# Kernel optimization log

Measured on AMD Instinct MI355X. Metric: run time of the kernel, lower is better.

The kernel has to match this reference:

```python
import jax, jax.numpy as jnp
import numpy as np

N = 50000        # num nodes
E = 800000       # num edges
F_IN = 128
H1 = 256
H2 = 256
C = 64


def _sage_conv(x, edge_index, W_l, b_l, W_r):
    """PyG SAGEConv (mean aggr): lin_l(mean over in-neighbors of x_j) + lin_r(x)."""
    src = edge_index[0]
    dst = edge_index[1]
    n = x.shape[0]
    # gather messages [E, d] then segment-mean into [N, d]
    agg = jax.ops.segment_sum(x[src], dst, num_segments=n)
    cnt = jax.ops.segment_sum(jnp.ones((edge_index.shape[1],), x.dtype), dst, num_segments=n)
    mean = agg / jnp.maximum(cnt, 1.0)[:, None]
    return mean @ W_l + b_l + x @ W_r


def setup_inputs() -> dict:
    key = jax.random.key(0)
    ks = jax.random.split(key, 10)
    x = jax.random.normal(ks[0], (N, F_IN), dtype=jnp.float32)
    edge_index = jax.random.randint(ks[1], (2, E), 0, N, dtype=jnp.int64)
    s1 = 1.0 / np.sqrt(F_IN)
    s2 = 1.0 / np.sqrt(H1)
    s3 = 1.0 / np.sqrt(H2)
    return {
        "x": x,
        "edge_index": edge_index,
        "W1_l": jax.random.uniform(ks[2], (F_IN, H1), jnp.float32, -s1, s1),
        "b1": jnp.zeros((H1,), jnp.float32),
        "W1_r": jax.random.uniform(ks[3], (F_IN, H1), jnp.float32, -s1, s1),
        "W2_l": jax.random.uniform(ks[4], (H1, H2), jnp.float32, -s2, s2),
        "b2": jnp.zeros((H2,), jnp.float32),
        "W2_r": jax.random.uniform(ks[5], (H1, H2), jnp.float32, -s2, s2),
        "Wc": jax.random.uniform(ks[6], (H2, C), jnp.float32, -s3, s3),
        "bc": jax.random.uniform(ks[7], (C,), jnp.float32, -s3, s3),
    }


def reference(x, edge_index, W1_l, b1, W1_r, W2_l, b2, W2_r, Wc, bc):
    # inference mode: dropout is identity
    h = jax.nn.relu(_sage_conv(x, edge_index, W1_l, b1, W1_r))
    h = jax.nn.relu(_sage_conv(h, edge_index, W2_l, b2, W2_r))
    return h @ Wc + bc
```

## Files before the change

kernel.cpp:

```cpp
#include <hip/hip_runtime.h>
#include <hip/hip_bf16.h>


#define F_IN 128
#define H1_DIM 256
#define H2_DIM 256
#define C_DIM 64

typedef __attribute__((ext_vector_type(8))) short bf16x8;
typedef __attribute__((ext_vector_type(8))) unsigned short u16x8;
typedef __attribute__((ext_vector_type(4))) float f32x4;

__device__ __forceinline__ unsigned short f2bf(float f) {
    unsigned u = __builtin_bit_cast(unsigned, f);
    u = (u + 0x7FFFu + ((u >> 16) & 1u)) >> 16;
    return (unsigned short)u;
}
__device__ __forceinline__ float bf2f(unsigned short h) {
    return __builtin_bit_cast(float, (unsigned)h << 16);
}

__global__ void k_detect(const unsigned int* __restrict__ ei, int* __restrict__ flag) {
    if (blockIdx.x == 0 && threadIdx.x == 0) {
        int is64 = 1;
        for (int i = 1; i < 256; i += 2) {
            if (ei[i] != 0u) { is64 = 0; break; }
        }
        *flag = is64;
    }
}

__device__ __forceinline__ int ei_at(const void* ei, const int* flag, long long idx) {
    return (*flag) ? (int)((const long long*)ei)[idx] : ((const int*)ei)[idx];
}

__global__ void k_degree(const void* __restrict__ ei, const int* __restrict__ flag,
                         int* __restrict__ cnt, int E) {
    int i = blockIdx.x * blockDim.x + threadIdx.x;
    if (i >= E) return;
    atomicAdd(&cnt[ei_at(ei, flag, (long long)E + i)], 1);
}

__global__ void k_scan1(const int* __restrict__ cnt, int* __restrict__ rowptr,
                        int* __restrict__ bsum, int n) {
    __shared__ int s[256];
    int i = blockIdx.x * 256 + threadIdx.x;
    int v = (i < n) ? cnt[i] : 0;
    s[threadIdx.x] = v;
    __syncthreads();
    for (int off = 1; off < 256; off <<= 1) {
        int t = (threadIdx.x >= off) ? s[threadIdx.x - off] : 0;
        __syncthreads();
        s[threadIdx.x] += t;
        __syncthreads();
    }
    if (i < n) rowptr[i] = s[threadIdx.x] - v;
    if (threadIdx.x == 255) bsum[blockIdx.x] = s[255];
}

__global__ void k_scan2(const int* __restrict__ bsum, int* __restrict__ boff, int nb) {
    __shared__ int s[1024];
    int t = threadIdx.x;
    int v = (t < nb) ? bsum[t] : 0;
    s[t] = v;
    __syncthreads();
    for (int off = 1; off < 1024; off <<= 1) {
        int u = (t >= off) ? s[t - off] : 0;
        __syncthreads();
        s[t] += u;
        __syncthreads();
    }
    if (t < nb) boff[t] = s[t] - v;
}

__global__ void k_scan3(int* __restrict__ rowptr, const int* __restrict__ boff,
                        int n, int total) {
    int i = blockIdx.x * 256 + threadIdx.x;
    if (i < n) rowptr[i] += boff[i >> 8];
    if (i == 0) rowptr[n] = total;
}

__global__ void k_scatter(const void* __restrict__ ei, const int* __restrict__ flag,
                          const int* __restrict__ rowptr, int* __restrict__ pos,
                          int* __restrict__ col, int E) {
    int i = blockIdx.x * blockDim.x + threadIdx.x;
    if (i >= E) return;
    int s = ei_at(ei, flag, i);
    int d = ei_at(ei, flag, (long long)E + i);
    int p = atomicAdd(&pos[d], 1);
    col[rowptr[d] + p] = s;
}

__global__ void k_prep_x(const float* __restrict__ x, unsigned short* __restrict__ hi,
                         unsigned short* __restrict__ lo, int n4) {
    int i = blockIdx.x * 256 + threadIdx.x;
    if (i >= n4) return;
    float4 v = ((const float4*)x)[i];
    ushort4 h, l;
    h.x = f2bf(v.x); l.x = f2bf(v.x - bf2f(h.x));
    h.y = f2bf(v.y); l.y = f2bf(v.y - bf2f(h.y));
    h.z = f2bf(v.z); l.z = f2bf(v.z - bf2f(h.z));
    h.w = f2bf(v.w); l.w = f2bf(v.w - bf2f(h.w));
    ((ushort4*)hi)[i] = h;
    ((ushort4*)lo)[i] = l;
}

struct WPrep {
    const float* W;
    unsigned short* hiT;
    unsigned short* loT;
    int K;
    int NN;
};

__global__ void k_prep_w(WPrep w0, WPrep w1, WPrep w2, WPrep w3, WPrep w4) {
    WPrep wp;
    switch (blockIdx.y) {
        case 0: wp = w0; break;
        case 1: wp = w1; break;
        case 2: wp = w2; break;
        case 3: wp = w3; break;
        default: wp = w4; break;
    }
    int total = wp.K * wp.NN;
    for (int i = blockIdx.x * 256 + threadIdx.x; i < total; i += gridDim.x * 256) {
        int k = i / wp.NN, n = i % wp.NN;
        float v = wp.W[i];
        unsigned short h = f2bf(v);
        wp.hiT[(size_t)n * wp.K + k] = h;
        wp.loT[(size_t)n * wp.K + k] = f2bf(v - bf2f(h));
    }
}

__global__ void k_agg1(const unsigned short* __restrict__ xhi,
                       const int* __restrict__ rowptr, const int* __restrict__ col,
                       unsigned short* __restrict__ mhi, unsigned short* __restrict__ mlo,
                       int n) {
    int w = blockIdx.x * 4 + (threadIdx.x >> 6);
    int lane = threadIdx.x & 63;
    if (w >= n) return;
    int q = lane >> 4;
    int ch = (lane & 15) * 8;
    int beg = rowptr[w], end = rowptr[w + 1];
    float inv = 1.0f / fmaxf((float)(end - beg), 1.0f);

    float a[8];
#pragma unroll
    for (int c = 0; c < 8; ++c) a[c] = 0.f;

    int j = beg + q;
    for (; j + 4 < end; j += 8) {
        int c0 = col[j], c1 = col[j + 4];
        u16x8 r0 = *(const u16x8*)(xhi + (size_t)c0 * 128 + ch);
        u16x8 r1 = *(const u16x8*)(xhi + (size_t)c1 * 128 + ch);
#pragma unroll
        for (int c = 0; c < 8; ++c) a[c] += bf2f(r0[c]) + bf2f(r1[c]);
    }
    if (j < end) {
        u16x8 r0 = *(const u16x8*)(xhi + (size_t)col[j] * 128 + ch);
#pragma unroll
        for (int c = 0; c < 8; ++c) a[c] += bf2f(r0[c]);
    }

#pragma unroll
    for (int c = 0; c < 8; ++c) a[c] += __shfl_xor(a[c], 16);
#pragma unroll
    for (int c = 0; c < 8; ++c) a[c] += __shfl_xor(a[c], 32);

    if (q < 2) {
        u16x8 o;
#pragma unroll
        for (int c = 0; c < 8; ++c) {
            float m = a[c] * inv;
            unsigned short h = f2bf(m);
            o[c] = (q == 0) ? h : f2bf(m - bf2f(h));
        }
        unsigned short* dst = (q == 0) ? mhi : mlo;
        *(u16x8*)(dst + (size_t)w * 128 + ch) = o;
    }
}

__global__ void k_agg2(const unsigned short* __restrict__ hhi,
                       const int* __restrict__ rowptr, const int* __restrict__ col,
                       unsigned short* __restrict__ mhi, unsigned short* __restrict__ mlo,
                       int n) {
    int w = blockIdx.x * 4 + (threadIdx.x >> 6);
    int lane = threadIdx.x & 63;
    if (w >= n) return;
    int h = lane >> 5;
    int ch = (lane & 31) * 8;
    int beg = rowptr[w], end = rowptr[w + 1];
    float inv = 1.0f / fmaxf((float)(end - beg), 1.0f);

    float a[8];
#pragma unroll
    for (int c = 0; c < 8; ++c) a[c] = 0.f;

    int j = beg + h;
    for (; j + 2 < end; j += 4) {
        int c0 = col[j], c1 = col[j + 2];
        u16x8 r0 = *(const u16x8*)(hhi + (size_t)c0 * 256 + ch);
        u16x8 r1 = *(const u16x8*)(hhi + (size_t)c1 * 256 + ch);
#pragma unroll
        for (int c = 0; c < 8; ++c) a[c] += bf2f(r0[c]) + bf2f(r1[c]);
    }
    if (j < end) {
        u16x8 r0 = *(const u16x8*)(hhi + (size_t)col[j] * 256 + ch);
#pragma unroll
        for (int c = 0; c < 8; ++c) a[c] += bf2f(r0[c]);
    }

#pragma unroll
    for (int c = 0; c < 8; ++c) a[c] += __shfl_xor(a[c], 32);

    u16x8 o;
#pragma unroll
    for (int c = 0; c < 8; ++c) {
        float m = a[c] * inv;
        unsigned short hh = f2bf(m);
        o[c] = (h == 0) ? hh : f2bf(m - bf2f(hh));
    }
    unsigned short* dst = (h == 0) ? mhi : mlo;
    *(u16x8*)(dst + (size_t)w * 256 + ch) = o;
}

struct Loads {
    const unsigned short* a[4];
    const unsigned short* b0[4];
    const unsigned short* b1[4];
};

template <int BN, int NLOAD, int KS, bool RELU, int OUTMODE>
__global__ __launch_bounds__(256, 3) void k_mfma_gemm(
    Loads L, const float* __restrict__ bias,
    float* __restrict__ Cf, unsigned short* __restrict__ Chi,
    unsigned short* __restrict__ Clo, int M, int NN) {
    constexpr int BM = 128;
    constexpr int WAVES = 4;
    constexpr int WCN = 2;
    constexpr int WRN = WAVES / WCN;
    constexpr int WM = BM / WRN;
    constexpr int WN = BN / WCN;
    constexpr int FM = WM / 16;
    constexpr int FN = WN / 16;
    constexpr int ACH = 16;
    constexpr int BCH = BN / 8;

    __shared__ unsigned short sA[BM * 64];
    __shared__ unsigned short sB[2][BN * 64];

    const int tid = threadIdx.x;
    const int lane = tid & 63;
    const int wid = tid >> 6;
    const int wr = wid / WCN, wc = wid % WCN;

    const int nbn = NN / BN;
    const int bm = (nbn == 1) ? blockIdx.x : blockIdx.x / nbn;
    const int bn = (nbn == 1) ? 0 : blockIdx.x % nbn;
    const int row0 = bm * BM;
    const int col0 = bn * BN;

    f32x4 acc[FM][FN];
#pragma unroll
    for (int m = 0; m < FM; ++m)
#pragma unroll
        for (int n = 0; n < FN; ++n) acc[m][n] = (f32x4){0.f, 0.f, 0.f, 0.f};

    const int l7 = lane & 7;
    const int l15 = lane & 15;
    const int q = lane >> 4;
    const int st_r = lane >> 3;
    const int st_k = 8 * (l7 ^ st_r);

    for (int ld = 0; ld < NLOAD; ++ld) {
        const unsigned short* Ag = L.a[ld];
        const unsigned short* B0 = L.b0[ld];
        const unsigned short* B1 = L.b1[ld];
        const bool dual = (B1 != nullptr);

        for (int k0 = 0; k0 < KS; k0 += 64) {
#pragma unroll
            for (int c = wid; c < ACH; c += WAVES) {
                int gr = row0 + c * 8 + st_r;
                if (gr >= M) gr = 0;
                const unsigned short* gp = Ag + (size_t)gr * KS + k0 + st_k;
                __builtin_amdgcn_global_load_lds(
                    (const __attribute__((address_space(1))) unsigned int*)gp,
                    (__attribute__((address_space(3))) unsigned int*)(sA + c * 512),
                    16, 0, 0);
            }
#pragma unroll
            for (int c = wid; c < BCH; c += WAVES) {
                int gn = col0 + c * 8 + st_r;
                const unsigned short* gp = B0 + (size_t)gn * KS + k0 + st_k;
                __builtin_amdgcn_global_load_lds(
                    (const __attribute__((address_space(1))) unsigned int*)gp,
                    (__attribute__((address_space(3))) unsigned int*)(sB[0] + c * 512),
                    16, 0, 0);
            }
            if (dual) {
#pragma unroll
                for (int c = wid; c < BCH; c += WAVES) {
                    int gn = col0 + c * 8 + st_r;
                    const unsigned short* gp = B1 + (size_t)gn * KS + k0 + st_k;
                    __builtin_amdgcn_global_load_lds(
                        (const __attribute__((address_space(1))) unsigned int*)gp,
                        (__attribute__((address_space(3))) unsigned int*)(sB[1] + c * 512),
                        16, 0, 0);
                }
            }
            __syncthreads();

#pragma unroll
            for (int ks = 0; ks < 2; ++ks) {
                const int sidx = 8 * ((q + 4 * ks) ^ l7);
                bf16x8 af[FM], b0f[FN], b1f[FN];
#pragma unroll
                for (int m = 0; m < FM; ++m) {
                    int rb = wr * WM + m * 16 + l15;
                    af[m] = *(const bf16x8*)(sA + (size_t)rb * 64 + sidx);
                }
#pragma unroll
                for (int n = 0; n < FN; ++n) {
                    int cb = wc * WN + n * 16 + l15;
                    b0f[n] = *(const bf16x8*)(sB[0] + (size_t)cb * 64 + sidx);
                }
                if (dual) {
#pragma unroll
                    for (int n = 0; n < FN; ++n) {
                        int cb = wc * WN + n * 16 + l15;
                        b1f[n] = *(const bf16x8*)(sB[1] + (size_t)cb * 64 + sidx);
                    }
                }
#pragma unroll
                for (int m = 0; m < FM; ++m)
#pragma unroll
                    for (int n = 0; n < FN; ++n)
                        acc[m][n] = __builtin_amdgcn_mfma_f32_16x16x32_bf16(
                            af[m], b0f[n], acc[m][n], 0, 0, 0);
                if (dual) {
#pragma unroll
                    for (int m = 0; m < FM; ++m)
#pragma unroll
                        for (int n = 0; n < FN; ++n)
                            acc[m][n] = __builtin_amdgcn_mfma_f32_16x16x32_bf16(
                                af[m], b1f[n], acc[m][n], 0, 0, 0);
                }
            }
            __syncthreads();
        }
    }

#pragma unroll
    for (int m = 0; m < FM; ++m) {
#pragma unroll
        for (int n = 0; n < FN; ++n) {
            int col = col0 + wc * WN + n * 16 + l15;
            float bb = bias[col];
#pragma unroll
            for (int r = 0; r < 4; ++r) {
                int row = row0 + wr * WM + m * 16 + q * 4 + r;
                if (row < M) {
                    float t = acc[m][n][r] + bb;
                    if (RELU) t = fmaxf(t, 0.f);
                    if (OUTMODE == 0) {
                        Cf[(size_t)row * NN + col] = t;
                    } else {
                        unsigned short hi = f2bf(t);
                        float lo = t - bf2f(hi);
                        Chi[(size_t)row * NN + col] = hi;
                        Clo[(size_t)row * NN + col] = f2bf(lo);
                    }
                }
            }
        }
    }
}

extern "C" void kernel_launch(void* const* d_in, const int* in_sizes, int n_in,
                              void* d_out, int out_size, void* d_ws, size_t ws_size,
                              hipStream_t stream) {
    const float* x   = (const float*)d_in[0];
    const void*  ei  = d_in[1];
    const float* W1l = (const float*)d_in[2];
    const float* b1  = (const float*)d_in[3];
    const float* W1r = (const float*)d_in[4];
    const float* W2l = (const float*)d_in[5];
    const float* b2  = (const float*)d_in[6];
    const float* W2r = (const float*)d_in[7];
    const float* Wc  = (const float*)d_in[8];
    const float* bc  = (const float*)d_in[9];
    float* out = (float*)d_out;

    const int N = in_sizes[0] / F_IN;
    const int E = in_sizes[1] / 2;

    typedef unsigned short u16;

    char* w = (char*)d_ws;
    size_t off = 0;
    auto carve = [&](size_t bytes) -> char* {
        char* p = w + off;
        off = (off + bytes + 255) & ~(size_t)255;
        return p;
    };
    int* cnt    = (int*)carve((size_t)N * 4);
    int* pos    = (int*)carve((size_t)N * 4);
    int* rowptr = (int*)carve((size_t)(N + 1) * 4);
    int* bsum   = (int*)carve(1024 * 4);
    int* boff   = (int*)carve(1024 * 4);
    int* flag   = (int*)carve(256);
    int* col    = (int*)carve((size_t)E * 4);

    u16* xhi    = (u16*)carve((size_t)N * F_IN * 2);
    u16* xlo    = (u16*)carve((size_t)N * F_IN * 2);
    u16* agghi  = (u16*)carve((size_t)N * 256 * 2);
    u16* agglo  = (u16*)carve((size_t)N * 256 * 2);
    u16* h1hi   = (u16*)carve((size_t)N * 256 * 2);
    u16* h1lo   = (u16*)carve((size_t)N * 256 * 2);
    u16* h2lo   = (u16*)carve((size_t)N * 256 * 2);
    u16* h2hi   = xhi;

    u16* w1l_hi = (u16*)carve((size_t)F_IN * H1_DIM * 2);
    u16* w1l_lo = (u16*)carve((size_t)F_IN * H1_DIM * 2);
    u16* w1r_hi = (u16*)carve((size_t)F_IN * H1_DIM * 2);
    u16* w1r_lo = (u16*)carve((size_t)F_IN * H1_DIM * 2);
    u16* w2l_hi = (u16*)carve((size_t)H1_DIM * H2_DIM * 2);
    u16* w2l_lo = (u16*)carve((size_t)H1_DIM * H2_DIM * 2);
    u16* w2r_hi = (u16*)carve((size_t)H1_DIM * H2_DIM * 2);
    u16* w2r_lo = (u16*)carve((size_t)H1_DIM * H2_DIM * 2);
    u16* wc_hi  = (u16*)carve((size_t)H2_DIM * C_DIM * 2);
    u16* wc_lo  = (u16*)carve((size_t)H2_DIM * C_DIM * 2);
    (void)ws_size;

    hipMemsetAsync(cnt, 0, (char*)rowptr - (char*)cnt, stream);

    k_detect<<<1, 64, 0, stream>>>((const unsigned int*)ei, flag);
    k_degree<<<(E + 255) / 256, 256, 0, stream>>>(ei, flag, cnt, E);
    int nb = (N + 255) / 256;
    k_scan1<<<nb, 256, 0, stream>>>(cnt, rowptr, bsum, N);
    k_scan2<<<1, 1024, 0, stream>>>(bsum, boff, nb);
    k_scan3<<<nb, 256, 0, stream>>>(rowptr, boff, N, E);
    k_scatter<<<(E + 255) / 256, 256, 0, stream>>>(ei, flag, rowptr, pos, col, E);

    k_prep_x<<<((N * F_IN / 4) + 255) / 256, 256, 0, stream>>>(x, xhi, xlo, N * F_IN / 4);
    {
        WPrep w0{W1l, w1l_hi, w1l_lo, F_IN, H1_DIM};
        WPrep w1{W1r, w1r_hi, w1r_lo, F_IN, H1_DIM};
        WPrep w2{W2l, w2l_hi, w2l_lo, H1_DIM, H2_DIM};
        WPrep w3{W2r, w2r_hi, w2r_lo, H1_DIM, H2_DIM};
        WPrep w4{Wc, wc_hi, wc_lo, H2_DIM, C_DIM};
        dim3 g(64, 5);
        k_prep_w<<<g, 256, 0, stream>>>(w0, w1, w2, w3, w4);
    }

    const int nbm = (N + 127) / 128;

    k_agg1<<<(N + 3) / 4, 256, 0, stream>>>(xhi, rowptr, col, agghi, agglo, N);
    {
        Loads L;
        L.a[0] = agghi; L.b0[0] = w1l_hi; L.b1[0] = w1l_lo;
        L.a[1] = agglo; L.b0[1] = w1l_hi; L.b1[1] = nullptr;
        L.a[2] = xhi;   L.b0[2] = w1r_hi; L.b1[2] = w1r_lo;
        L.a[3] = xlo;   L.b0[3] = w1r_hi; L.b1[3] = nullptr;
        k_mfma_gemm<128, 4, 128, true, 1><<<nbm * (H1_DIM / 128), 256, 0, stream>>>(
            L, b1, nullptr, h1hi, h1lo, N, H1_DIM);
    }

    k_agg2<<<(N + 3) / 4, 256, 0, stream>>>(h1hi, rowptr, col, agghi, agglo, N);
    {
        Loads L;
        L.a[0] = agghi; L.b0[0] = w2l_hi; L.b1[0] = w2l_lo;
        L.a[1] = agglo; L.b0[1] = w2l_hi; L.b1[1] = nullptr;
        L.a[2] = h1hi;  L.b0[2] = w2r_hi; L.b1[2] = w2r_lo;
        L.a[3] = h1lo;  L.b0[3] = w2r_hi; L.b1[3] = nullptr;
        k_mfma_gemm<128, 4, 256, true, 1><<<nbm * (H2_DIM / 128), 256, 0, stream>>>(
            L, b2, nullptr, h2hi, h2lo, N, H2_DIM);
    }

    {
        Loads L;
        L.a[0] = h2hi; L.b0[0] = wc_hi; L.b1[0] = wc_lo;
        L.a[1] = h2lo; L.b0[1] = wc_hi; L.b1[1] = nullptr;
        L.a[2] = nullptr; L.b0[2] = nullptr; L.b1[2] = nullptr;
        L.a[3] = nullptr; L.b0[3] = nullptr; L.b1[3] = nullptr;
        k_mfma_gemm<64, 2, 256, false, 0><<<nbm, 256, 0, stream>>>(
            L, bc, out, nullptr, nullptr, N, C_DIM);
    }
}
```

Measured before the change: 405.8 us.

## Replace split-bf16 hi/lo emulation with single fp16 operands throughout

Drops the three-term bf16 hi/lo split used to emulate fp32 precision and stores activations, aggregated means and weights as a single fp16 copy, using fp16 MFMA. This removes the lo buffers, halves the GEMM load passes, removes the extra MFMA passes, and shrinks the memory traffic of preparation, aggregation and epilogue writes. It also raises launch bounds occupancy to 4 now that the second B buffer in LDS is gone. The risk is lower accuracy and fp16 range limits on intermediate values compared with the near-fp32 emulation.

```diff
diff --git a/kernel.cpp b/kernel.cpp
--- a/kernel.cpp
+++ b/kernel.cpp
@@ -7,17 +7,15 @@
 #define H2_DIM 256
 #define C_DIM 64
 
-typedef __attribute__((ext_vector_type(8))) short bf16x8;
+typedef __attribute__((ext_vector_type(8))) _Float16 f16x8;
 typedef __attribute__((ext_vector_type(8))) unsigned short u16x8;
 typedef __attribute__((ext_vector_type(4))) float f32x4;
 
-__device__ __forceinline__ unsigned short f2bf(float f) {
-    unsigned u = __builtin_bit_cast(unsigned, f);
-    u = (u + 0x7FFFu + ((u >> 16) & 1u)) >> 16;
-    return (unsigned short)u;
-}
-__device__ __forceinline__ float bf2f(unsigned short h) {
-    return __builtin_bit_cast(float, (unsigned)h << 16);
+__device__ __forceinline__ unsigned short f2h(float f) {
+    return __builtin_bit_cast(unsigned short, (_Float16)f);
+}
+__device__ __forceinline__ float h2f(unsigned short h) {
+    return (float)__builtin_bit_cast(_Float16, h);
 }
 
 __global__ void k_detect(const unsigned int* __restrict__ ei, int* __restrict__ flag) {
@@ -91,24 +89,22 @@
     col[rowptr[d] + p] = s;
 }
 
-__global__ void k_prep_x(const float* __restrict__ x, unsigned short* __restrict__ hi,
-                         unsigned short* __restrict__ lo, int n4) {
+__global__ void k_prep_x(const float* __restrict__ x, unsigned short* __restrict__ xh,
+                         int n4) {
     int i = blockIdx.x * 256 + threadIdx.x;
     if (i >= n4) return;
     float4 v = ((const float4*)x)[i];
-    ushort4 h, l;
-    h.x = f2bf(v.x); l.x = f2bf(v.x - bf2f(h.x));
-    h.y = f2bf(v.y); l.y = f2bf(v.y - bf2f(h.y));
-    h.z = f2bf(v.z); l.z = f2bf(v.z - bf2f(h.z));
-    h.w = f2bf(v.w); l.w = f2bf(v.w - bf2f(h.w));
-    ((ushort4*)hi)[i] = h;
-    ((ushort4*)lo)[i] = l;
+    ushort4 h;
+    h.x = f2h(v.x);
+    h.y = f2h(v.y);
+    h.z = f2h(v.z);
+    h.w = f2h(v.w);
+    ((ushort4*)xh)[i] = h;
 }
 
 struct WPrep {
     const float* W;
-    unsigned short* hiT;
-    unsigned short* loT;
+    unsigned short* wT;
     int K;
     int NN;
 };
@@ -125,17 +121,13 @@
     int total = wp.K * wp.NN;
     for (int i = blockIdx.x * 256 + threadIdx.x; i < total; i += gridDim.x * 256) {
         int k = i / wp.NN, n = i % wp.NN;
-        float v = wp.W[i];
-        unsigned short h = f2bf(v);
-        wp.hiT[(size_t)n * wp.K + k] = h;
-        wp.loT[(size_t)n * wp.K + k] = f2bf(v - bf2f(h));
-    }
-}
-
-__global__ void k_agg1(const unsigned short* __restrict__ xhi,
+        wp.wT[(size_t)n * wp.K + k] = f2h(wp.W[i]);
+    }
+}
+
+__global__ void k_agg1(const unsigned short* __restrict__ xh,
                        const int* __restrict__ rowptr, const int* __restrict__ col,
-                       unsigned short* __restrict__ mhi, unsigned short* __restrict__ mlo,
-                       int n) {
+                       unsigned short* __restrict__ mean, int n) {
     int w = blockIdx.x * 4 + (threadIdx.x >> 6);
     int lane = threadIdx.x & 63;
     if (w >= n) return;
@@ -151,15 +143,15 @@
     int j = beg + q;
     for (; j + 4 < end; j += 8) {
         int c0 = col[j], c1 = col[j + 4];
-        u16x8 r0 = *(const u16x8*)(xhi + (size_t)c0 * 128 + ch);
-        u16x8 r1 = *(const u16x8*)(xhi + (size_t)c1 * 128 + ch);
-#pragma unroll
-        for (int c = 0; c < 8; ++c) a[c] += bf2f(r0[c]) + bf2f(r1[c]);
+        u16x8 r0 = *(const u16x8*)(xh + (size_t)c0 * 128 + ch);
+        u16x8 r1 = *(const u16x8*)(xh + (size_t)c1 * 128 + ch);
+#pragma unroll
+        for (int c = 0; c < 8; ++c) a[c] += h2f(r0[c]) + h2f(r1[c]);
     }
     if (j < end) {
-        u16x8 r0 = *(const u16x8*)(xhi + (size_t)col[j] * 128 + ch);
-#pragma unroll
-        for (int c = 0; c < 8; ++c) a[c] += bf2f(r0[c]);
+        u16x8 r0 = *(const u16x8*)(xh + (size_t)col[j] * 128 + ch);
+#pragma unroll
+        for (int c = 0; c < 8; ++c) a[c] += h2f(r0[c]);
     }
 
 #pragma unroll
@@ -167,23 +159,17 @@
 #pragma unroll
     for (int c = 0; c < 8; ++c) a[c] += __shfl_xor(a[c], 32);
 
-    if (q < 2) {
+    if (q == 0) {
         u16x8 o;
 #pragma unroll
-        for (int c = 0; c < 8; ++c) {
-            float m = a[c] * inv;
-            unsigned short h = f2bf(m);
-            o[c] = (q == 0) ? h : f2bf(m - bf2f(h));
-        }
-        unsigned short* dst = (q == 0) ? mhi : mlo;
-        *(u16x8*)(dst + (size_t)w * 128 + ch) = o;
-    }
-}
-
-__global__ void k_agg2(const unsigned short* __restrict__ hhi,
+        for (int c = 0; c < 8; ++c) o[c] = f2h(a[c] * inv);
+        *(u16x8*)(mean + (size_t)w * 128 + ch) = o;
+    }
+}
+
+__global__ void k_agg2(const unsigned short* __restrict__ hh,
                        const int* __restrict__ rowptr, const int* __restrict__ col,
-                       unsigned short* __restrict__ mhi, unsigned short* __restrict__ mlo,
-                       int n) {
+                       unsigned short* __restrict__ mean, int n) {
     int w = blockIdx.x * 4 + (threadIdx.x >> 6);
     int lane = threadIdx.x & 63;
     if (w >= n) return;
@@ -199,55 +185,49 @@
     int j = beg + h;
     for (; j + 2 < end; j += 4) {
         int c0 = col[j], c1 = col[j + 2];
-        u16x8 r0 = *(const u16x8*)(hhi + (size_t)c0 * 256 + ch);
-        u16x8 r1 = *(const u16x8*)(hhi + (size_t)c1 * 256 + ch);
-#pragma unroll
-        for (int c = 0; c < 8; ++c) a[c] += bf2f(r0[c]) + bf2f(r1[c]);
+        u16x8 r0 = *(const u16x8*)(hh + (size_t)c0 * 256 + ch);
+        u16x8 r1 = *(const u16x8*)(hh + (size_t)c1 * 256 + ch);
+#pragma unroll
+        for (int c = 0; c < 8; ++c) a[c] += h2f(r0[c]) + h2f(r1[c]);
     }
     if (j < end) {
-        u16x8 r0 = *(const u16x8*)(hhi + (size_t)col[j] * 256 + ch);
-#pragma unroll
-        for (int c = 0; c < 8; ++c) a[c] += bf2f(r0[c]);
+        u16x8 r0 = *(const u16x8*)(hh + (size_t)col[j] * 256 + ch);
+#pragma unroll
+        for (int c = 0; c < 8; ++c) a[c] += h2f(r0[c]);
     }
 
 #pragma unroll
     for (int c = 0; c < 8; ++c) a[c] += __shfl_xor(a[c], 32);
 
-    u16x8 o;
-#pragma unroll
-    for (int c = 0; c < 8; ++c) {
-        float m = a[c] * inv;
-        unsigned short hh = f2bf(m);
-        o[c] = (h == 0) ? hh : f2bf(m - bf2f(hh));
-    }
-    unsigned short* dst = (h == 0) ? mhi : mlo;
-    *(u16x8*)(dst + (size_t)w * 256 + ch) = o;
+    if (h == 0) {
+        u16x8 o;
+#pragma unroll
+        for (int c = 0; c < 8; ++c) o[c] = f2h(a[c] * inv);
+        *(u16x8*)(mean + (size_t)w * 256 + ch) = o;
+    }
 }
 
 struct Loads {
-    const unsigned short* a[4];
-    const unsigned short* b0[4];
-    const unsigned short* b1[4];
+    const unsigned short* a[2];
+    const unsigned short* b[2];
 };
 
 template <int BN, int NLOAD, int KS, bool RELU, int OUTMODE>
-__global__ __launch_bounds__(256, 3) void k_mfma_gemm(
+__global__ __launch_bounds__(256, 4) void k_mfma_gemm(
     Loads L, const float* __restrict__ bias,
-    float* __restrict__ Cf, unsigned short* __restrict__ Chi,
-    unsigned short* __restrict__ Clo, int M, int NN) {
+    float* __restrict__ Cf, unsigned short* __restrict__ Ch, int M, int NN) {
     constexpr int BM = 128;
     constexpr int WAVES = 4;
     constexpr int WCN = 2;
-    constexpr int WRN = WAVES / WCN;
-    constexpr int WM = BM / WRN;
+    constexpr int WM = 64;
     constexpr int WN = BN / WCN;
-    constexpr int FM = WM / 16;
+    constexpr int FM = 4;
     constexpr int FN = WN / 16;
     constexpr int ACH = 16;
     constexpr int BCH = BN / 8;
 
     __shared__ unsigned short sA[BM * 64];
-    __shared__ unsigned short sB[2][BN * 64];
+    __shared__ unsigned short sB[BN * 64];
 
     const int tid = threadIdx.x;
     const int lane = tid & 63;
@@ -274,9 +254,7 @@
 
     for (int ld = 0; ld < NLOAD; ++ld) {
         const unsigned short* Ag = L.a[ld];
-        const unsigned short* B0 = L.b0[ld];
-        const unsigned short* B1 = L.b1[ld];
-        const bool dual = (B1 != nullptr);
+        const unsigned short* Bg = L.b[ld];
 
         for (int k0 = 0; k0 < KS; k0 += 64) {
 #pragma unroll
@@ -292,60 +270,34 @@
 #pragma unroll
             for (int c = wid; c < BCH; c += WAVES) {
                 int gn = col0 + c * 8 + st_r;
-                const unsigned short* gp = B0 + (size_t)gn * KS + k0 + st_k;
+                const unsigned short* gp = Bg + (size_t)gn * KS + k0 + st_k;
                 __builtin_amdgcn_global_load_lds(
                     (const __attribute__((address_space(1))) unsigned int*)gp,
-                    (__attribute__((address_space(3))) unsigned int*)(sB[0] + c * 512),
+                    (__attribute__((address_space(3))) unsigned int*)(sB + c * 512),
                     16, 0, 0);
             }
-            if (dual) {
-#pragma unroll
-                for (int c = wid; c < BCH; c += WAVES) {
-                    int gn = col0 + c * 8 + st_r;
-                    const unsigned short* gp = B1 + (size_t)gn * KS + k0 + st_k;
-                    __builtin_amdgcn_global_load_lds(
-                        (const __attribute__((address_space(1))) unsigned int*)gp,
-                        (__attribute__((address_space(3))) unsigned int*)(sB[1] + c * 512),
-                        16, 0, 0);
-                }
-            }
             __syncthreads();
 
 #pragma unroll
             for (int ks = 0; ks < 2; ++ks) {
                 const int sidx = 8 * ((q + 4 * ks) ^ l7);
-                bf16x8 af[FM], b0f[FN], b1f[FN];
+                f16x8 af[FM], bf[FN];
 #pragma unroll
                 for (int m = 0; m < FM; ++m) {
                     int rb = wr * WM + m * 16 + l15;
-                    af[m] = *(const bf16x8*)(sA + (size_t)rb * 64 + sidx);
+                    af[m] = *(const f16x8*)(sA + (size_t)rb * 64 + sidx);
                 }
 #pragma unroll
                 for (int n = 0; n < FN; ++n) {
                     int cb = wc * WN + n * 16 + l15;
-                    b0f[n] = *(const bf16x8*)(sB[0] + (size_t)cb * 64 + sidx);
+                    bf[n] = *(const f16x8*)(sB + (size_t)cb * 64 + sidx);
                 }
-                if (dual) {
-#pragma unroll
-                    for (int n = 0; n < FN; ++n) {
-                        int cb = wc * WN + n * 16 + l15;
-                        b1f[n] = *(const bf16x8*)(sB[1] + (size_t)cb * 64 + sidx);
-                    }
-                }
 #pragma unroll
                 for (int m = 0; m < FM; ++m)
 #pragma unroll
                     for (int n = 0; n < FN; ++n)
-                        acc[m][n] = __builtin_amdgcn_mfma_f32_16x16x32_bf16(
-                            af[m], b0f[n], acc[m][n], 0, 0, 0);
-                if (dual) {
-#pragma unroll
-                    for (int m = 0; m < FM; ++m)
-#pragma unroll
-                        for (int n = 0; n < FN; ++n)
-                            acc[m][n] = __builtin_amdgcn_mfma_f32_16x16x32_bf16(
-                                af[m], b1f[n], acc[m][n], 0, 0, 0);
-                }
+                        acc[m][n] = __builtin_amdgcn_mfma_f32_16x16x32_f16(
+                            af[m], bf[n], acc[m][n], 0, 0, 0);
             }
             __syncthreads();
         }
@@ -366,10 +318,7 @@
                     if (OUTMODE == 0) {
                         Cf[(size_t)row * NN + col] = t;
                     } else {
-                        unsigned short hi = f2bf(t);
-                        float lo = t - bf2f(hi);
-                        Chi[(size_t)row * NN + col] = hi;
-                        Clo[(size_t)row * NN + col] = f2bf(lo);
+                        Ch[(size_t)row * NN + col] = f2h(t);
                     }
                 }
             }
@@ -412,25 +361,16 @@
     int* flag   = (int*)carve(256);
     int* col    = (int*)carve((size_t)E * 4);
 
-    u16* xhi    = (u16*)carve((size_t)N * F_IN * 2);
-    u16* xlo    = (u16*)carve((size_t)N * F_IN * 2);
-    u16* agghi  = (u16*)carve((size_t)N * 256 * 2);
-    u16* agglo  = (u16*)carve((size_t)N * 256 * 2);
-    u16* h1hi   = (u16*)carve((size_t)N * 256 * 2);
-    u16* h1lo   = (u16*)carve((size_t)N * 256 * 2);
-    u16* h2lo   = (u16*)carve((size_t)N * 256 * 2);
-    u16* h2hi   = xhi;
-
-    u16* w1l_hi = (u16*)carve((size_t)F_IN * H1_DIM * 2);
-    u16* w1l_lo = (u16*)carve((size_t)F_IN * H1_DIM * 2);
-    u16* w1r_hi = (u16*)carve((size_t)F_IN * H1_DIM * 2);
-    u16* w1r_lo = (u16*)carve((size_t)F_IN * H1_DIM * 2);
-    u16* w2l_hi = (u16*)carve((size_t)H1_DIM * H2_DIM * 2);
-    u16* w2l_lo = (u16*)carve((size_t)H1_DIM * H2_DIM * 2);
-    u16* w2r_hi = (u16*)carve((size_t)H1_DIM * H2_DIM * 2);
-    u16* w2r_lo = (u16*)carve((size_t)H1_DIM * H2_DIM * 2);
-    u16* wc_hi  = (u16*)carve((size_t)H2_DIM * C_DIM * 2);
-    u16* wc_lo  = (u16*)carve((size_t)H2_DIM * C_DIM * 2);
+    u16* xh     = (u16*)carve((size_t)N * F_IN * 2);
+    u16* agg    = (u16*)carve((size_t)N * 256 * 2);
+    u16* h1     = (u16*)carve((size_t)N * 256 * 2);
+    u16* h2     = (u16*)carve((size_t)N * 256 * 2);
+
+    u16* w1lT   = (u16*)carve((size_t)F_IN * H1_DIM * 2);
+    u16* w1rT   = (u16*)carve((size_t)F_IN * H1_DIM * 2);
+    u16* w2lT   = (u16*)carve((size_t)H1_DIM * H2_DIM * 2);
+    u16* w2rT   = (u16*)carve((size_t)H1_DIM * H2_DIM * 2);
+    u16* wcT    = (u16*)carve((size_t)H2_DIM * C_DIM * 2);
     (void)ws_size;
 
     hipMemsetAsync(cnt, 0, (char*)rowptr - (char*)cnt, stream);
@@ -443,48 +383,42 @@
     k_scan3<<<nb, 256, 0, stream>>>(rowptr, boff, N, E);
     k_scatter<<<(E + 255) / 256, 256, 0, stream>>>(ei, flag, rowptr, pos, col, E);
 
-    k_prep_x<<<((N * F_IN / 4) + 255) / 256, 256, 0, stream>>>(x, xhi, xlo, N * F_IN / 4);
+    k_prep_x<<<((N * F_IN / 4) + 255) / 256, 256, 0, stream>>>(x, xh, N * F_IN / 4);
     {
-        WPrep w0{W1l, w1l_hi, w1l_lo, F_IN, H1_DIM};
-        WPrep w1{W1r, w1r_hi, w1r_lo, F_IN, H1_DIM};
-        WPrep w2{W2l, w2l_hi, w2l_lo, H1_DIM, H2_DIM};
-        WPrep w3{W2r, w2r_hi, w2r_lo, H1_DIM, H2_DIM};
-        WPrep w4{Wc, wc_hi, wc_lo, H2_DIM, C_DIM};
+        WPrep w0{W1l, w1lT, F_IN, H1_DIM};
+        WPrep w1{W1r, w1rT, F_IN, H1_DIM};
+        WPrep w2{W2l, w2lT, H1_DIM, H2_DIM};
+        WPrep w3{W2r, w2rT, H1_DIM, H2_DIM};
+        WPrep w4{Wc, wcT, H2_DIM, C_DIM};
         dim3 g(64, 5);
         k_prep_w<<<g, 256, 0, stream>>>(w0, w1, w2, w3, w4);
     }
 
     const int nbm = (N + 127) / 128;
 
-    k_agg1<<<(N + 3) / 4, 256, 0, stream>>>(xhi, rowptr, col, agghi, agglo, N);
+    k_agg1<<<(N + 3) / 4, 256, 0, stream>>>(xh, rowptr, col, agg, N);
     {
         Loads L;
-        L.a[0] = agghi; L.b0[0] = w1l_hi; L.b1[0] = w1l_lo;
-        L.a[1] = agglo; L.b0[1] = w1l_hi; L.b1[1] = nullptr;
-        L.a[2] = xhi;   L.b0[2] = w1r_hi; L.b1[2] = w1r_lo;
-        L.a[3] = xlo;   L.b0[3] = w1r_hi; L.b1[3] = nullptr;
-        k_mfma_gemm<128, 4, 128, true, 1><<<nbm * (H1_DIM / 128), 256, 0, stream>>>(
-            L, b1, nullptr, h1hi, h1lo, N, H1_DIM);
-    }
-
-    k_agg2<<<(N + 3) / 4, 256, 0, stream>>>(h1hi, rowptr, col, agghi, agglo, N);
+        L.a[0] = agg; L.b[0] = w1lT;
+        L.a[1] = xh;  L.b[1] = w1rT;
+        k_mfma_gemm<128, 2, 128, true, 1><<<nbm * (H1_DIM / 128), 256, 0, stream>>>(
+            L, b1, nullptr, h1, N, H1_DIM);
+    }
+
+    k_agg2<<<(N + 3) / 4, 256, 0, stream>>>(h1, rowptr, col, agg, N);
     {
         Loads L;
-        L.a[0] = agghi; L.b0[0] = w2l_hi; L.b1[0] = w2l_lo;
-        L.a[1] = agglo; L.b0[1] = w2l_hi; L.b1[1] = nullptr;
-        L.a[2] = h1hi;  L.b0[2] = w2r_hi; L.b1[2] = w2r_lo;
-        L.a[3] = h1lo;  L.b0[3] = w2r_hi; L.b1[3] = nullptr;
-        k_mfma_gemm<128, 4, 256, true, 1><<<nbm * (H2_DIM / 128), 256, 0, stream>>>(
-            L, b2, nullptr, h2hi, h2lo, N, H2_DIM);
+        L.a[0] = agg; L.b[0] = w2lT;
+        L.a[1] = h1;  L.b[1] = w2rT;
+        k_mfma_gemm<128, 2, 256, true, 1><<<nbm * (H2_DIM / 128), 256, 0, stream>>>(
+            L, b2, nullptr, h2, N, H2_DIM);
     }
 
     {
         Loads L;
-        L.a[0] = h2hi; L.b0[0] = wc_hi; L.b1[0] = wc_lo;
-        L.a[1] = h2lo; L.b0[1] = wc_hi; L.b1[1] = nullptr;
-        L.a[2] = nullptr; L.b0[2] = nullptr; L.b1[2] = nullptr;
-        L.a[3] = nullptr; L.b0[3] = nullptr; L.b1[3] = nullptr;
-        k_mfma_gemm<64, 2, 256, false, 0><<<nbm, 256, 0, stream>>>(
-            L, bc, out, nullptr, nullptr, N, C_DIM);
-    }
-}
+        L.a[0] = h2; L.b[0] = wcT;
+        L.a[1] = nullptr; L.b[1] = nullptr;
+        k_mfma_gemm<64, 1, 256, false, 0><<<nbm, 256, 0, stream>>>(
+            L, bc, out, nullptr, N, C_DIM);
+    }
+}
```

Measured after the change: 334.8 us. -17.5%, faster.
